# Performance work log

Measured on AMD Instinct MI355X. Metric: run time of the kernel, lower is better.

Reference implementation:

```python
import jax, jax.numpy as jnp
import numpy as np

V = 500000   # num_vertexes
T = 4        # edge_type_num
D = 32       # edge_embedding_size
E = 128      # embedding_size
A = 32       # attention_dim
B = 8192     # batch
S = 10       # neighbor_samples


def setup_inputs() -> dict:
    key = jax.random.key(0)
    ks = jax.random.split(key, 8)
    glorot = lambda k, shape: jax.random.normal(k, shape, dtype=jnp.float32) * np.sqrt(2.0 / (shape[-2] + shape[-1])).astype(np.float32)
    return {
        "targets": jax.random.randint(ks[0], (B,), 0, V, dtype=jnp.int32),
        "types": jax.random.randint(ks[1], (B,), 0, T, dtype=jnp.int32),
        "neighbors": jax.random.randint(ks[2], (B, T, S), 0, V, dtype=jnp.int32),
        "base_node_embeddings": jax.random.uniform(ks[3], (V, E), minval=-1.0, maxval=1.0, dtype=jnp.float32),
        "node_type_embeddings": jax.random.uniform(ks[4], (V, T, D), minval=-1.0, maxval=1.0, dtype=jnp.float32),
        "trans_weights": glorot(ks[5], (T, D, E)),
        "trans_weights_s1": glorot(ks[6], (T, D, A)),
        "trans_weights_s2": glorot(ks[7], (T, A, 1)),
    }


def reference(targets, types, neighbors,
              base_node_embeddings, node_type_embeddings,
              trans_weights, trans_weights_s1, trans_weights_s2):
    # TF code gathers [B,T,S,T,D] then slices the (i,i) diagonal per edge type.
    # Equivalent, cheaper: per edge type i, gather node_type_embeddings[:, i, :]
    # at neighbors[:, i, :].  vmap over the edge-type axis.
    nte_t = jnp.transpose(node_type_embeddings, (1, 0, 2))          # [T,V,D]
    gathered = jax.vmap(lambda emb_t, nb_t: emb_t[nb_t],
                        in_axes=(0, 1))(nte_t, neighbors)           # [T,B,S,D]
    node_agg = jnp.transpose(gathered.mean(axis=2), (1, 0, 2))      # [B,T,D]

    tw  = trans_weights[types]       # [B,D,E]
    tw1 = trans_weights_s1[types]    # [B,D,A]
    tw2 = trans_weights_s2[types]    # [B,A,1]

    u = jnp.tanh(jnp.einsum('btd,bda->bta', node_agg, tw1))         # [B,T,A]
    scores = jnp.einsum('bta,bao->bto', u, tw2)[..., 0]             # [B,T]
    att = jax.nn.softmax(scores, axis=-1)                           # [B,T]
    node_att = jnp.einsum('bt,btd->bd', att, node_agg)              # [B,D]
    proj = jnp.einsum('bd,bde->be', node_att, tw)                   # [B,E]

    all_node_embed = base_node_embeddings[targets] + proj           # [B,E]
    # tf.nn.l2_normalize: x * rsqrt(max(sum(x^2), 1e-12))
    sq = jnp.sum(all_node_embed * all_node_embed, axis=1, keepdims=True)
    embeddings = all_node_embed * jax.lax.rsqrt(jnp.maximum(sq, 1e-12))
    return embeddings
```

## Files before the change

kernel.cpp:

```cpp
#include <hip/hip_runtime.h>
#include <hip/hip_bf16.h>


constexpr int TT = 4;
constexpr int DD = 32;
constexpr int EE = 128;
constexpr int AA = 32;
constexpr int SS = 10;

__global__ __launch_bounds__(128) void gatne_fused(
    const int*   __restrict__ targets,
    const int*   __restrict__ types,
    const int*   __restrict__ neighbors,
    const float* __restrict__ base_emb,
    const float* __restrict__ nte,
    const float* __restrict__ tw,
    const float* __restrict__ tw1,
    const float* __restrict__ tw2,
    float*       __restrict__ out)
{
    const int b    = blockIdx.x;
    const int tid  = threadIdx.x;
    const int t    = tid >> 5;
    const int lane = tid & 31;

    __shared__ float s_agg[TT][DD];
    __shared__ float s_scores[TT];
    __shared__ float s_natt[DD];
    __shared__ int   s_nb[TT * SS];
    __shared__ int   s_meta[2];
    __shared__ float s_part[2];
    __shared__ float s_inv;

    if (tid == 0) s_meta[0] = types[b];
    if (tid == 1) s_meta[1] = targets[b];
    if (tid < TT * SS) s_nb[tid] = neighbors[b * (TT * SS) + tid];
    __syncthreads();

    const int ty = s_meta[0];
    const int tg = s_meta[1];

    float acc = 0.f;
    #pragma unroll
    for (int s = 0; s < SS; ++s) {
        const int v = s_nb[t * SS + s];
        acc += nte[(long long)v * (TT * DD) + t * DD + lane];
    }
    s_agg[t][lane] = acc * 0.1f;
    __syncthreads();

    float ua = 0.f;
    #pragma unroll
    for (int d = 0; d < DD; ++d)
        ua += s_agg[t][d] * tw1[ty * (DD * AA) + d * AA + lane];
    ua = tanhf(ua);

    float p = ua * tw2[ty * AA + lane];
    #pragma unroll
    for (int m = 16; m >= 1; m >>= 1)
        p += __shfl_xor(p, m, 64);
    if (lane == 0) s_scores[t] = p;
    __syncthreads();

    const float sc0 = s_scores[0], sc1 = s_scores[1];
    const float sc2 = s_scores[2], sc3 = s_scores[3];
    const float mx  = fmaxf(fmaxf(sc0, sc1), fmaxf(sc2, sc3));
    const float e0 = expf(sc0 - mx), e1 = expf(sc1 - mx);
    const float e2 = expf(sc2 - mx), e3 = expf(sc3 - mx);
    const float inv_sum = 1.f / (e0 + e1 + e2 + e3);

    if (tid < DD) {
        const float na = (e0 * s_agg[0][tid] + e1 * s_agg[1][tid] +
                          e2 * s_agg[2][tid] + e3 * s_agg[3][tid]) * inv_sum;
        s_natt[tid] = na;
    }
    __syncthreads();

    float val = 0.f;
    #pragma unroll
    for (int d = 0; d < DD; ++d)
        val += s_natt[d] * tw[ty * (DD * EE) + d * EE + tid];
    val += base_emb[(long long)tg * EE + tid];

    float sq = val * val;
    #pragma unroll
    for (int m = 32; m >= 1; m >>= 1)
        sq += __shfl_xor(sq, m, 64);
    if ((tid & 63) == 0) s_part[tid >> 6] = sq;
    __syncthreads();
    if (tid == 0) s_inv = rsqrtf(fmaxf(s_part[0] + s_part[1], 1e-12f));
    __syncthreads();

    out[b * EE + tid] = val * s_inv;
}

extern "C" void kernel_launch(void* const* d_in, const int* in_sizes, int n_in,
                              void* d_out, int out_size, void* d_ws, size_t ws_size,
                              hipStream_t stream) {
    const int*   targets   = (const int*)d_in[0];
    const int*   types     = (const int*)d_in[1];
    const int*   neighbors = (const int*)d_in[2];
    const float* base_emb  = (const float*)d_in[3];
    const float* nte       = (const float*)d_in[4];
    const float* tw        = (const float*)d_in[5];
    const float* tw1       = (const float*)d_in[6];
    const float* tw2       = (const float*)d_in[7];
    float*       out       = (float*)d_out;

    const int B = in_sizes[0];
    (void)n_in; (void)out_size; (void)d_ws; (void)ws_size;

    gatne_fused<<<B, 128, 0, stream>>>(targets, types, neighbors,
                                       base_emb, nte, tw, tw1, tw2, out);
}
```

Baseline: 413.0 us.

## Split neighbor gather into separate high-occupancy kernel writing aggregates to workspace

Moves the random neighbor gather-and-mean out of the fused kernel into its own kernel, with 256-thread blocks that each handle 8 (batch, type) groups and load neighbor indices straight into registers. The aggregates go to workspace and a second epilogue kernel does the attention, projection and normalization. The epilogue also issues the base embedding load early so it overlaps the remaining work. The aim is more memory-level parallelism on the latency-bound gather, at the cost of an extra launch and a workspace round trip of B*T*D floats.

New measurement: 416.0 us. About the same (+0.7%).

```diff
diff --git a/kernel.cpp b/kernel.cpp
--- a/kernel.cpp
+++ b/kernel.cpp
@@ -1,5 +1,4 @@
 #include <hip/hip_runtime.h>
-#include <hip/hip_bf16.h>
 
 
 constexpr int TT = 4;
@@ -8,12 +7,33 @@
 constexpr int AA = 32;
 constexpr int SS = 10;
 
-__global__ __launch_bounds__(128) void gatne_fused(
+__global__ __launch_bounds__(256, 8) void gatne_agg(
+    const int*   __restrict__ neighbors,
+    const float* __restrict__ nte,
+    float*       __restrict__ agg)
+{
+    const int g    = blockIdx.x * 8 + (threadIdx.x >> 5);
+    const int lane = threadIdx.x & 31;
+    const int t    = g & (TT - 1);
+
+    const int* nbp = neighbors + (long long)g * SS;
+    int vs[SS];
+    #pragma unroll
+    for (int s = 0; s < SS; ++s) vs[s] = nbp[s];
+
+    float acc = 0.f;
+    #pragma unroll
+    for (int s = 0; s < SS; ++s)
+        acc += nte[(long long)vs[s] * (TT * DD) + t * DD + lane];
+
+    agg[(long long)g * DD + lane] = acc * 0.1f;
+}
+
+__global__ __launch_bounds__(128) void gatne_epilogue(
     const int*   __restrict__ targets,
     const int*   __restrict__ types,
-    const int*   __restrict__ neighbors,
+    const float* __restrict__ agg,
     const float* __restrict__ base_emb,
-    const float* __restrict__ nte,
     const float* __restrict__ tw,
     const float* __restrict__ tw1,
     const float* __restrict__ tw2,
@@ -27,26 +47,16 @@
     __shared__ float s_agg[TT][DD];
     __shared__ float s_scores[TT];
     __shared__ float s_natt[DD];
-    __shared__ int   s_nb[TT * SS];
-    __shared__ int   s_meta[2];
     __shared__ float s_part[2];
     __shared__ float s_inv;
 
-    if (tid == 0) s_meta[0] = types[b];
-    if (tid == 1) s_meta[1] = targets[b];
-    if (tid < TT * SS) s_nb[tid] = neighbors[b * (TT * SS) + tid];
-    __syncthreads();
+    const int ty = types[b];
+    const int tg = targets[b];
 
-    const int ty = s_meta[0];
-    const int tg = s_meta[1];
+    const float base_v = base_emb[(long long)tg * EE + tid];
 
-    float acc = 0.f;
-    #pragma unroll
-    for (int s = 0; s < SS; ++s) {
-        const int v = s_nb[t * SS + s];
-        acc += nte[(long long)v * (TT * DD) + t * DD + lane];
-    }
-    s_agg[t][lane] = acc * 0.1f;
+    const float agg_mine = agg[((long long)b * TT + t) * DD + lane];
+    s_agg[t][lane] = agg_mine;
     __syncthreads();
 
     float ua = 0.f;
@@ -80,7 +90,7 @@
     #pragma unroll
     for (int d = 0; d < DD; ++d)
         val += s_natt[d] * tw[ty * (DD * EE) + d * EE + tid];
-    val += base_emb[(long long)tg * EE + tid];
+    val += base_v;
 
     float sq = val * val;
     #pragma unroll
@@ -106,10 +116,12 @@
     const float* tw1       = (const float*)d_in[6];
     const float* tw2       = (const float*)d_in[7];
     float*       out       = (float*)d_out;
+    float*       agg       = (float*)d_ws;
 
     const int B = in_sizes[0];
-    (void)n_in; (void)out_size; (void)d_ws; (void)ws_size;
+    (void)n_in; (void)out_size; (void)ws_size;
 
-    gatne_fused<<<B, 128, 0, stream>>>(targets, types, neighbors,
-                                       base_emb, nte, tw, tw1, tw2, out);
+    gatne_agg<<<(B * TT) / 8, 256, 0, stream>>>(neighbors, nte, agg);
+    gatne_epilogue<<<B, 128, 0, stream>>>(targets, types, agg, base_emb,
+                                          tw, tw1, tw2, out);
 }
```
